# Kernel tuning notes

Measured on AMD Instinct MI355X. Metric: run time of the kernel, lower is better.

The kernel has to match this reference:

```python
import jax, jax.numpy as jnp
import numpy as np

H = 12          # num attention heads
DH = 64         # head size (768 / 12)
THRESHOLD = 0.05


def setup_inputs() -> dict:
    key = jax.random.key(0)
    ks = jax.random.split(key, 13)
    B, S, D = 128, 197, 768
    s = 0.02
    return {
        "hidden_states": jax.random.normal(ks[0], (B, S, D), jnp.float32),
        "Wq": jax.random.normal(ks[1], (D, D), jnp.float32) * s,
        "bq": jax.random.normal(ks[2], (D,), jnp.float32) * s,
        "Wk": jax.random.normal(ks[3], (D, D), jnp.float32) * s,
        "bk": jax.random.normal(ks[4], (D,), jnp.float32) * s,
        "Wv": jax.random.normal(ks[5], (D, D), jnp.float32) * s,
        "bv": jax.random.normal(ks[6], (D,), jnp.float32) * s,
        "Wd": jax.random.normal(ks[7], (D, D), jnp.float32) * s,
        "bd": jax.random.normal(ks[8], (D,), jnp.float32) * s,
        "W1": jax.random.normal(ks[9], (D, 64), jnp.float32) * s,
        "b1": jax.random.normal(ks[10], (64,), jnp.float32) * s,
        "W2": jax.random.normal(ks[11], (64, 1), jnp.float32) * s,
        "b2": jax.random.normal(ks[12], (1,), jnp.float32) * s,
    }


def reference(hidden_states, Wq, bq, Wk, bk, Wv, bv, Wd, bd, W1, b1, W2, b2):
    B, S, D = hidden_states.shape
    # --- DHS scoring MLP on patch tokens (exclude CLS), keep_cls=True path ---
    h = jax.nn.relu(hidden_states[:, 1:] @ W1 + b1)        # [B, S-1, 64]
    mlp_out = jax.nn.sigmoid(h @ W2 + b2)[..., 0]          # [B, S-1]
    patch_mask = mlp_out >= THRESHOLD                      # [B, S-1]
    cls_col = jnp.ones((B, 1), dtype=bool)
    mask = jnp.concatenate([cls_col, patch_mask], axis=1)  # [B, S]

    # --- full self-attention; pruning queries only removes rows, keys/values
    # are never pruned, so computing all rows and masking is equivalent ---
    q = (hidden_states @ Wq + bq).reshape(B, S, H, DH)
    k = (hidden_states @ Wk + bk).reshape(B, S, H, DH)
    v = (hidden_states @ Wv + bv).reshape(B, S, H, DH)
    scores = jnp.einsum("bqhd,bkhd->bhqk", q, k) / jnp.sqrt(jnp.float32(DH))
    probs = jax.nn.softmax(scores, axis=-1)                # dropout p=0.0 (eval)
    ctx = jnp.einsum("bhqk,bkhd->bqhd", probs, v).reshape(B, S, D)
    attn_out = (ctx @ Wd + bd) + ctx                       # dense + residual-to-self_outputs

    # scatter-assign: output[i][mask[i]] = attn_out rows for kept tokens
    output = jnp.where(mask[..., None], attn_out, hidden_states)
    return output
```

## Files before the change

### kernel.cpp

```cpp
#include <hip/hip_runtime.h>
#include <hip/hip_bf16.h>

#define HN 12
#define DHD 64
#define BB 128
#define SQ 197
#define DD 768
#define TOK (BB*SQ)
#define SP 224
#define SPS 232

using short8  = __attribute__((ext_vector_type(8))) short;
using floatx4 = __attribute__((ext_vector_type(4))) float;

__device__ __forceinline__ float bf2f(short v) {
    union { unsigned int u; float f; } x;
    x.u = ((unsigned int)(unsigned short)v) << 16;
    return x.f;
}
__device__ __forceinline__ short f2bf(float f) {
    union { float f; unsigned int u; } x; x.f = f;
    unsigned int u = x.u;
    u += 0x7fffu + ((u >> 16) & 1u);
    return (short)(u >> 16);
}
__device__ __forceinline__ float ldf(const void* p, size_t i, bool isf32) {
    return isf32 ? ((const float*)p)[i] : bf2f(((const short*)p)[i]);
}
__device__ __forceinline__ void gload_lds16(const short* g, short* l) {
    __builtin_amdgcn_global_load_lds(
        (const __attribute__((address_space(1))) void*)g,
        (__attribute__((address_space(3))) void*)l, 16, 0, 0);
}

__global__ __launch_bounds__(256) void detect_kernel(
        const short* __restrict__ wq, float* __restrict__ flag) {
    __shared__ int cnt;
    if (threadIdx.x == 0) cnt = 0;
    __syncthreads();
    int local = 0;
    for (int j = 0; j < 16; j++) {
        int i = threadIdx.x * 16 + j;
        unsigned int u = (unsigned short)wq[2 * i];
        unsigned int e = (u >> 7) & 0xFF;
        if (e < 64 || e >= 192) local++;
    }
    for (int d = 1; d < 64; d <<= 1) local += __shfl_xor(local, d, 64);
    if ((threadIdx.x & 63) == 0) atomicAdd(&cnt, local);
    __syncthreads();
    if (threadIdx.x == 0) *flag = (cnt > 256) ? 1.f : 0.f;
}

__global__ void sentinel_kernel(short* out, int n, float code) {
    int i = blockIdx.x * 256 + threadIdx.x;
    if (i < n) out[i] = (i == 0) ? f2bf(code) : (short)0;
}

__global__ __launch_bounds__(256) void prep_kernel(
        const void* __restrict__ Wq, const void* __restrict__ Wk,
        const void* __restrict__ Wv, const void* __restrict__ Wd,
        const void* __restrict__ bq, const void* __restrict__ bk,
        const void* __restrict__ bv, const void* __restrict__ bd,
        const void* __restrict__ W1, const void* __restrict__ b1,
        const void* __restrict__ W2, const void* __restrict__ b2,
        short* __restrict__ WqkvT, short* __restrict__ WdT,
        short* __restrict__ W1T, float* __restrict__ bcat,
        const float* __restrict__ flag) {
    __shared__ short tile[64][72];
    bool isf32 = (*flag != 0.f);
    int blk = blockIdx.x;
    int tid = threadIdx.x;
    int r = tid >> 2, c0 = (tid & 3) << 4;
    const void* W;
    size_t stride;
    int ti, tj, w = 0;
    if (blk < 576) {
        w = blk / 144;
        int t = blk % 144;
        ti = t / 12; tj = t % 12;
        W = (w == 0) ? Wq : (w == 1) ? Wk : (w == 2) ? Wv : Wd;
        stride = DD;
    } else {
        ti = blk - 576; tj = 0;
        W = W1;
        stride = 64;
    }
    for (int c = 0; c < 16; c++)
        tile[r][c0 + c] =
            f2bf(ldf(W, (size_t)(ti * 64 + r) * stride + tj * 64 + c0 + c, isf32));
    __syncthreads();
    short* out;
    if (blk < 576)
        out = (w < 3)
            ? WqkvT + ((size_t)(w * DD + tj * 64 + r)) * DD + ti * 64
            : WdT   + ((size_t)(tj * 64 + r)) * DD + ti * 64;
    else
        out = W1T + (size_t)r * DD + ti * 64;
    for (int h = 0; h < 2; h++) {
        short8 v;
        #pragma unroll
        for (int c = 0; c < 8; c++) v[c] = tile[c0 + h * 8 + c][r];
        *(short8*)&out[c0 + h * 8] = v;
    }
    if (blk == 0) {
        for (int i = tid; i < DD; i += 256) {
            bcat[i]          = ldf(bq, i, isf32);
            bcat[DD + i]     = ldf(bk, i, isf32);
            bcat[2 * DD + i] = ldf(bv, i, isf32);
            bcat[3 * DD + i] = ldf(bd, i, isf32);
        }
        if (tid < 64) {
            bcat[4 * DD + tid]      = ldf(b1, tid, isf32);
            bcat[4 * DD + 64 + tid] = ldf(W2, tid, isf32);
        }
        if (tid == 0) bcat[4 * DD + 128] = ldf(b2, 0, isf32);
    }
}

__global__ __launch_bounds__(256) void mask_gemm(
        const void* __restrict__ hs, const short* __restrict__ W1T,
        const float* __restrict__ bvec, float* __restrict__ mask,
        short* __restrict__ hsb, const float* __restrict__ flag) {
    __shared__ __align__(16) short As[64 * 32];
    __shared__ __align__(16) short Bs[64 * 32];
    bool isf32 = (*flag != 0.f);
    int tid = threadIdx.x, lane = tid & 63, wave = tid >> 6;
    int quad = lane >> 4, l16 = lane & 15;
    int tok0 = blockIdx.x * 64;

    int arow = tid >> 2, achk = tid & 3;
    int acol = ((achk ^ ((arow >> 1) & 3)) << 3);
    const short* Bg = W1T + (size_t)arow * DD +
                      (((achk ^ ((arow >> 1) & 3)) << 3));
    short* Bl = Bs + wave * 512;
    int fcol = ((quad ^ ((l16 >> 1) & 3)) << 3);

    floatx4 acc[4] = {};
    for (int k0 = 0; k0 < DD; k0 += 32) {
        gload_lds16(Bg + k0, Bl);
        size_t gidx = (size_t)(tok0 + arow) * DD + k0 + achk * 8;
        short8 s;
        if (isf32) {
            const float* hf = (const float*)hs;
            float4 f0 = *(const float4*)&hf[gidx];
            float4 f1 = *(const float4*)&hf[gidx + 4];
            s[0]=f2bf(f0.x); s[1]=f2bf(f0.y); s[2]=f2bf(f0.z); s[3]=f2bf(f0.w);
            s[4]=f2bf(f1.x); s[5]=f2bf(f1.y); s[6]=f2bf(f1.z); s[7]=f2bf(f1.w);
        } else {
            s = *(const short8*)&((const short*)hs)[gidx];
        }
        *(short8*)&hsb[gidx] = s;
        *(short8*)&As[(arow << 5) + acol] = s;
        __syncthreads();
        short8 af = *(const short8*)&As[((wave * 16 + l16) << 5) + fcol];
        #pragma unroll
        for (int j = 0; j < 4; j++) {
            short8 bf8 = *(const short8*)&Bs[((j * 16 + l16) << 5) + fcol];
            acc[j] = __builtin_amdgcn_mfma_f32_16x16x32_bf16(af, bf8, acc[j], 0, 0, 0);
        }
        __syncthreads();
    }

    const float* b1f = bvec + 4 * DD;
    const float* w2f = bvec + 4 * DD + 64;
    float b2v = bvec[4 * DD + 128];
    float partial[4] = {0.f, 0.f, 0.f, 0.f};
    #pragma unroll
    for (int j = 0; j < 4; j++) {
        int n = j * 16 + l16;
        float b1v = b1f[n], w2v = w2f[n];
        #pragma unroll
        for (int r = 0; r < 4; r++) {
            float hv = fmaxf(acc[j][r] + b1v, 0.f);
            partial[r] += hv * w2v;
        }
    }
    for (int d = 1; d < 16; d <<= 1)
        #pragma unroll
        for (int r = 0; r < 4; r++)
            partial[r] += __shfl_xor(partial[r], d, 64);
    if (l16 == 0) {
        #pragma unroll
        for (int r = 0; r < 4; r++) {
            int tokr = tok0 + wave * 16 + quad * 4 + r;
            float m = 1.f;
            if (tokr % SQ != 0) {
                float sg = 1.f / (1.f + __expf(-(partial[r] + b2v)));
                m = (sg >= 0.05f) ? 1.f : 0.f;
            }
            mask[tokr] = m;
        }
    }
}

template <int MODE>
__global__ __launch_bounds__(256) void gemm128(
        const short* __restrict__ A, const short* __restrict__ BT,
        const float* __restrict__ bias, void* __restrict__ C,
        int m0g, int Mreal, int N,
        const float* __restrict__ mask, const short* __restrict__ resid,
        const void* __restrict__ hs, const float* __restrict__ flag) {
    constexpr int K = DD;
    __shared__ __align__(16) short As[128 * 32];
    __shared__ __align__(16) short Bs[128 * 32];
    int tiles_n = N >> 7;
    int nwg = gridDim.x, bid = blockIdx.x;
    int qq = nwg >> 3, rr = nwg & 7, xcd = bid & 7, lid = bid >> 3;
    int wg = (xcd < rr ? xcd * (qq + 1) : rr * (qq + 1) + (xcd - rr) * qq) + lid;
    int bm = wg / tiles_n, bn = wg % tiles_n;
    int m0 = bm << 7, n0 = bn << 7;

    int tid = threadIdx.x, lane = tid & 63, wave = tid >> 6;
    int wx = wave & 1, wy = wave >> 1;
    int quad = lane >> 4, l16 = lane & 15;

    int s0 = tid, s1 = 256 + tid;
    int ar0 = s0 >> 2, ac0 = ((s0 & 3) ^ ((ar0 >> 1) & 3)) << 3;
    int ar1 = s1 >> 2, ac1 = ((s1 & 3) ^ ((ar1 >> 1) & 3)) << 3;
    int am0 = m0 + ar0; if (am0 >= Mreal) am0 = Mreal - 1;
    int am1 = m0 + ar1; if (am1 >= Mreal) am1 = Mreal - 1;
    const short* Ag0 = A + (size_t)am0 * K + ac0;
    const short* Ag1 = A + (size_t)am1 * K + ac1;
    const short* Bg0 = BT + (size_t)(n0 + ar0) * K + ac0;
    const short* Bg1 = BT + (size_t)(n0 + ar1) * K + ac1;
    short* Al0 = As + wave * 512;
    short* Al1 = As + 2048 + wave * 512;
    short* Bl0 = Bs + wave * 512;
    short* Bl1 = Bs + 2048 + wave * 512;

    int acol = ((quad ^ ((l16 >> 1) & 3)) << 3);

    floatx4 acc[4][4] = {};
    for (int k0 = 0; k0 < K; k0 += 32) {
        gload_lds16(Ag0 + k0, Al0);
        gload_lds16(Ag1 + k0, Al1);
        gload_lds16(Bg0 + k0, Bl0);
        gload_lds16(Bg1 + k0, Bl1);
        __syncthreads();
        short8 af[4], bfr[4];
        #pragma unroll
        for (int i = 0; i < 4; i++) {
            int row = (wy << 6) + (i << 4) + l16;
            af[i] = *(const short8*)&As[(row << 5) + acol];
        }
        #pragma unroll
        for (int j = 0; j < 4; j++) {
            int row = (wx << 6) + (j << 4) + l16;
            bfr[j] = *(const short8*)&Bs[(row << 5) + acol];
        }
        #pragma unroll
        for (int i = 0; i < 4; i++)
            #pragma unroll
            for (int j = 0; j < 4; j++)
                acc[i][j] = __builtin_amdgcn_mfma_f32_16x16x32_bf16(
                    af[i], bfr[j], acc[i][j], 0, 0, 0);
        __syncthreads();
    }

    bool isf32 = (MODE == 1) ? (*flag != 0.f) : false;
    #pragma unroll
    for (int i = 0; i < 4; i++)
        #pragma unroll
        for (int j = 0; j < 4; j++) {
            int n = n0 + (wx << 6) + (j << 4) + l16;
            float bb = bias[n];
            #pragma unroll
            for (int r = 0; r < 4; r++) {
                int m = m0 + (wy << 6) + (i << 4) + (quad << 2) + r;
                if (m >= Mreal) continue;
                float v = acc[i][j][r] + bb;
                if (MODE == 0) {
                    ((short*)C)[(size_t)m * N + n] = f2bf(v);
                } else {
                    size_t gm = (size_t)(m0g + m);
                    v += bf2f(resid[(size_t)m * N + n]);
                    if (mask[gm] == 0.f) v = ldf(hs, gm * N + n, isf32);
                    if (isf32) ((float*)C)[gm * N + n] = v;
                    else       ((short*)C)[gm * N + n] = f2bf(v);
                }
            }
        }
}

__global__ __launch_bounds__(256) void attn_kernel(
        const short* __restrict__ qkv, short* __restrict__ ctx) {
    __shared__ __align__(16) short Vt[DHD * SPS];
    __shared__ __align__(16) short P[4 * 16 * SPS];
    int blk = blockIdx.x;
    int qc = blk & 3;
    int h  = (blk >> 2) % HN;
    int b  = blk / (4 * HN);
    int tid = threadIdx.x, lane = tid & 63, wave = tid >> 6;
    int quad = lane >> 4, l16 = lane & 15;
    const short* base = qkv + (size_t)b * SQ * 2304;

    for (int i = tid; i < SQ * DHD; i += 256) {
        int s = i >> 6, d = i & 63;
        Vt[d * SPS + s] = base[(size_t)s * 2304 + 1536 + h * 64 + d];
    }
    for (int i = tid; i < (SP - SQ) * DHD; i += 256) {
        int s = SQ + i % (SP - SQ), d = i / (SP - SQ);
        Vt[d * SPS + s] = 0;
    }
    __syncthreads();

    int mrow = qc * 64 + wave * 16 + l16;
    if (mrow > SQ - 1) mrow = SQ - 1;
    const short* Qrow = base + (size_t)mrow * 2304 + h * 64;
    short8 aq0 = *(const short8*)(Qrow + quad * 8);
    short8 aq1 = *(const short8*)(Qrow + 32 + quad * 8);

    floatx4 sc[14];
    for (int t = 0; t < 14; t++) {
        int nrow = t * 16 + l16;
        if (nrow > SQ - 1) nrow = SQ - 1;
        const short* Krow = base + (size_t)nrow * 2304 + DD + h * 64;
        short8 b0 = *(const short8*)(Krow + quad * 8);
        short8 b1 = *(const short8*)(Krow + 32 + quad * 8);
        floatx4 c = {0.f, 0.f, 0.f, 0.f};
        c = __builtin_amdgcn_mfma_f32_16x16x32_bf16(aq0, b0, c, 0, 0, 0);
        c = __builtin_amdgcn_mfma_f32_16x16x32_bf16(aq1, b1, c, 0, 0, 0);
        sc[t] = c;
    }

    const float scale = 0.125f;
    float mx[4] = {-1e30f, -1e30f, -1e30f, -1e30f};
    for (int t = 0; t < 14; t++) {
        int col = t * 16 + l16;
        if (col < SQ)
            for (int r = 0; r < 4; r++) mx[r] = fmaxf(mx[r], sc[t][r]);
    }
    for (int d = 1; d < 16; d <<= 1)
        for (int r = 0; r < 4; r++) mx[r] = fmaxf(mx[r], __shfl_xor(mx[r], d, 64));
    float sum[4] = {0.f, 0.f, 0.f, 0.f};
    for (int t = 0; t < 14; t++) {
        int col = t * 16 + l16;
        for (int r = 0; r < 4; r++) {
            float e = (col < SQ) ? __expf((sc[t][r] - mx[r]) * scale) : 0.f;
            sc[t][r] = e; sum[r] += e;
        }
    }
    for (int d = 1; d < 16; d <<= 1)
        for (int r = 0; r < 4; r++) sum[r] += __shfl_xor(sum[r], d, 64);
    float inv[4];
    for (int r = 0; r < 4; r++) inv[r] = 1.f / sum[r];

    short* Pw = &P[wave * 16 * SPS];
    for (int t = 0; t < 14; t++)
        for (int r = 0; r < 4; r++)
            Pw[(quad * 4 + r) * SPS + t * 16 + l16] = f2bf(sc[t][r] * inv[r]);
    __syncthreads();

    floatx4 co[4] = {};
    for (int ks = 0; ks < 7; ks++) {
        short8 pa = *(const short8*)&Pw[l16 * SPS + ks * 32 + quad * 8];
        for (int j = 0; j < 4; j++) {
            short8 vb = *(const short8*)&Vt[(j * 16 + l16) * SPS + ks * 32 + quad * 8];
            co[j] = __builtin_amdgcn_mfma_f32_16x16x32_bf16(pa, vb, co[j], 0, 0, 0);
        }
    }
    int sq0 = qc * 64 + wave * 16 + quad * 4;
    for (int r = 0; r < 4; r++) {
        int s = sq0 + r;
        if (s < SQ) {
            size_t o = ((size_t)(b * SQ + s)) * DD + h * 64;
            for (int j = 0; j < 4; j++)
                ctx[o + j * 16 + l16] = f2bf(co[j][r]);
        }
    }
}

extern "C" void kernel_launch(void* const* d_in, const int* in_sizes, int n_in,
                              void* d_out, int out_size, void* d_ws, size_t ws_size,
                              hipStream_t stream) {
    const void* hs = d_in[0];
    const void* Wq = d_in[1];
    const void* bq = d_in[2];
    const void* Wk = d_in[3];
    const void* bk = d_in[4];
    const void* Wv = d_in[5];
    const void* bv = d_in[6];
    const void* Wd = d_in[7];
    const void* bd = d_in[8];
    const void* W1 = d_in[9];
    const void* b1 = d_in[10];
    const void* W2 = d_in[11];
    const void* b2 = d_in[12];

    const size_t flag_b  = 16;
    const size_t mask_b  = (size_t)TOK * 4;
    const size_t bcat_b  = (size_t)(4 * DD + 192) * 4;
    const size_t wqkvt_b = (size_t)3 * DD * DD * 2;
    const size_t wdt_b   = (size_t)DD * DD * 2;
    const size_t w1t_b   = (size_t)64 * DD * 2;
    const size_t hsb_b   = (size_t)TOK * DD * 2;
    const size_t fixed   = flag_b + mask_b + bcat_b + wqkvt_b + wdt_b + w1t_b + hsb_b;

    int CHB = 0;
    for (int c = 128; c >= 1; c >>= 1) {
        size_t chtp = (size_t)((c * SQ + 127) / 128) * 128;
        size_t need = fixed + chtp * 2304 * 2 + chtp * DD * 2;
        if (need <= ws_size) { CHB = c; break; }
    }
    if (CHB == 0) {
        sentinel_kernel<<<(out_size + 255) / 256, 256, 0, stream>>>(
            (short*)d_out, out_size, (float)((double)ws_size / 1.0e6));
        return;
    }
    const int CHT  = CHB * SQ;
    const int CHTP = ((CHT + 127) / 128) * 128;

    char* ws = (char*)d_ws;
    float* flag  = (float*)ws;
    float* mask  = (float*)(ws + flag_b);
    float* bcat  = (float*)(ws + flag_b + mask_b);
    short* WqkvT = (short*)(ws + flag_b + mask_b + bcat_b);
    short* WdT   = WqkvT + (size_t)3 * DD * DD;
    short* W1T   = WdT + (size_t)DD * DD;
    short* hsb   = W1T + (size_t)64 * DD;
    short* QKVc  = hsb + (size_t)TOK * DD;
    short* ctxc  = QKVc + (size_t)CHTP * 2304;

    detect_kernel<<<1, 256, 0, stream>>>((const short*)Wq, flag);
    prep_kernel<<<588, 256, 0, stream>>>(Wq, Wk, Wv, Wd, bq, bk, bv, bd,
                                         W1, b1, W2, b2,
                                         WqkvT, WdT, W1T, bcat, flag);
    mask_gemm<<<TOK / 64, 256, 0, stream>>>(hs, W1T, bcat, mask, hsb, flag);

    const int nchunk  = BB / CHB;
    const int tiles_m = CHTP / 128;
    for (int c = 0; c < nchunk; c++) {
        const int m0g = c * CHT;
        gemm128<0><<<tiles_m * (3 * DD / 128), 256, 0, stream>>>(
            hsb + (size_t)m0g * DD, WqkvT, bcat, QKVc,
            m0g, CHT, 3 * DD, nullptr, nullptr, nullptr, flag);
        attn_kernel<<<CHB * HN * 4, 256, 0, stream>>>(QKVc, ctxc);
        gemm128<1><<<tiles_m * (DD / 128), 256, 0, stream>>>(
            ctxc, WdT, bcat + 3 * DD, d_out,
            m0g, CHT, DD, mask, ctxc, hs, flag);
    }
}
```

Measured before the change: 625.3 us.

## Double-buffer GEMM LDS tiles and remap attention blocks per XCD

The GEMM main loop now uses two LDS buffers and prefetches the next K-slice with direct global-to-LDS loads while the MFMAs run on the current slice. This drops one barrier per iteration and hides load latency. It also raises wave priority around the MFMA block and precomputes the LDS row offsets. The attention kernel gets the same XCD-aware block remap already used by the GEMM, so blocks of the same batch share an L2. The cost is double the GEMM LDS footprint, which may reduce occupancy.

```diff
diff --git a/kernel.cpp b/kernel.cpp
--- a/kernel.cpp
+++ b/kernel.cpp
@@ -201,8 +201,9 @@
         const float* __restrict__ mask, const short* __restrict__ resid,
         const void* __restrict__ hs, const float* __restrict__ flag) {
     constexpr int K = DD;
-    __shared__ __align__(16) short As[128 * 32];
-    __shared__ __align__(16) short Bs[128 * 32];
+    constexpr int NT = K / 32;
+    __shared__ __align__(16) short As[2 * 128 * 32];
+    __shared__ __align__(16) short Bs[2 * 128 * 32];
     int tiles_n = N >> 7;
     int nwg = gridDim.x, bid = blockIdx.x;
     int qq = nwg >> 3, rr = nwg & 7, xcd = bid & 7, lid = bid >> 3;
@@ -229,32 +230,59 @@
     short* Bl1 = Bs + 2048 + wave * 512;
 
     int acol = ((quad ^ ((l16 >> 1) & 3)) << 3);
+    int arowA[4], arowB[4];
+    #pragma unroll
+    for (int i = 0; i < 4; i++) {
+        arowA[i] = (((wy << 6) + (i << 4) + l16) << 5) + acol;
+        arowB[i] = (((wx << 6) + (i << 4) + l16) << 5) + acol;
+    }
 
     floatx4 acc[4][4] = {};
-    for (int k0 = 0; k0 < K; k0 += 32) {
-        gload_lds16(Ag0 + k0, Al0);
-        gload_lds16(Ag1 + k0, Al1);
-        gload_lds16(Bg0 + k0, Bl0);
-        gload_lds16(Bg1 + k0, Bl1);
-        __syncthreads();
+    gload_lds16(Ag0, Al0);
+    gload_lds16(Ag1, Al1);
+    gload_lds16(Bg0, Bl0);
+    gload_lds16(Bg1, Bl1);
+    __syncthreads();
+    int cur = 0;
+    for (int t = 0; t < NT - 1; ++t) {
+        int kn = (t + 1) << 5;
+        int nxt = cur ^ 1;
+        gload_lds16(Ag0 + kn, Al0 + nxt * 4096);
+        gload_lds16(Ag1 + kn, Al1 + nxt * 4096);
+        gload_lds16(Bg0 + kn, Bl0 + nxt * 4096);
+        gload_lds16(Bg1 + kn, Bl1 + nxt * 4096);
+        const short* Ab = As + cur * 4096;
+        const short* Bb = Bs + cur * 4096;
         short8 af[4], bfr[4];
         #pragma unroll
-        for (int i = 0; i < 4; i++) {
-            int row = (wy << 6) + (i << 4) + l16;
-            af[i] = *(const short8*)&As[(row << 5) + acol];
-        }
-        #pragma unroll
-        for (int j = 0; j < 4; j++) {
-            int row = (wx << 6) + (j << 4) + l16;
-            bfr[j] = *(const short8*)&Bs[(row << 5) + acol];
-        }
+        for (int i = 0; i < 4; i++) af[i]  = *(const short8*)&Ab[arowA[i]];
+        #pragma unroll
+        for (int j = 0; j < 4; j++) bfr[j] = *(const short8*)&Bb[arowB[j]];
+        __builtin_amdgcn_s_setprio(1);
         #pragma unroll
         for (int i = 0; i < 4; i++)
             #pragma unroll
             for (int j = 0; j < 4; j++)
                 acc[i][j] = __builtin_amdgcn_mfma_f32_16x16x32_bf16(
                     af[i], bfr[j], acc[i][j], 0, 0, 0);
+        __builtin_amdgcn_s_setprio(0);
         __syncthreads();
+        cur = nxt;
+    }
+    {
+        const short* Ab = As + cur * 4096;
+        const short* Bb = Bs + cur * 4096;
+        short8 af[4], bfr[4];
+        #pragma unroll
+        for (int i = 0; i < 4; i++) af[i]  = *(const short8*)&Ab[arowA[i]];
+        #pragma unroll
+        for (int j = 0; j < 4; j++) bfr[j] = *(const short8*)&Bb[arowB[j]];
+        #pragma unroll
+        for (int i = 0; i < 4; i++)
+            #pragma unroll
+            for (int j = 0; j < 4; j++)
+                acc[i][j] = __builtin_amdgcn_mfma_f32_16x16x32_bf16(
+                    af[i], bfr[j], acc[i][j], 0, 0, 0);
     }
 
     bool isf32 = (MODE == 1) ? (*flag != 0.f) : false;
@@ -286,7 +314,9 @@
         const short* __restrict__ qkv, short* __restrict__ ctx) {
     __shared__ __align__(16) short Vt[DHD * SPS];
     __shared__ __align__(16) short P[4 * 16 * SPS];
-    int blk = blockIdx.x;
+    int nwg = gridDim.x, bid = blockIdx.x;
+    int qq = nwg >> 3, rr = nwg & 7, xcd = bid & 7, lid = bid >> 3;
+    int blk = (xcd < rr ? xcd * (qq + 1) : rr * (qq + 1) + (xcd - rr) * qq) + lid;
     int qc = blk & 3;
     int h  = (blk >> 2) % HN;
     int b  = blk / (4 * HN);
```

Result: no change. 618.3 us (-1.1%).
